# Optimization experiments

Measured on AMD Instinct MI355X. Metric: run time of the kernel, lower is better.

The kernel has to match this reference:

```python
import jax, jax.numpy as jnp
import numpy as np

L, B, F, E, H, V, NL, K = 32, 128, 4096, 512, 512, 50000, 2, 20


def setup_inputs() -> dict:
    key = jax.random.key(0)
    ks = jax.random.split(key, 9)
    return {
        "dialog_encoder_inputs": jax.random.randint(ks[0], (L, B), 0, V),
        "fact_inputs": jax.random.normal(ks[1], (B, F, E), dtype=jnp.float32),
        "h": jax.random.normal(ks[2], (NL, B, H), dtype=jnp.float32),
        "c": jax.random.normal(ks[3], (NL, B, H), dtype=jnp.float32),
        "enc_emb": jax.random.normal(ks[4], (V, E), dtype=jnp.float32) * 0.02,
        "Aw": jax.random.normal(ks[5], (H, E), dtype=jnp.float32) * 0.04,
        "Ab": jnp.zeros((H,), dtype=jnp.float32),
        "Cw": jax.random.normal(ks[6], (H, E), dtype=jnp.float32) * 0.04,
        "Cb": jnp.zeros((H,), dtype=jnp.float32),
        "top_k": K,
    }


def reference(dialog_encoder_inputs, fact_inputs, h, c, enc_emb, Aw, Ab, Cw, Cb, top_k):
    # --- get_top_k_fact_average: embed dialog, score facts, gather top-k ---
    q = enc_emb[dialog_encoder_inputs].mean(axis=0)                # [B, E] mean-pooled query
    scores = jnp.einsum('be,bfe->bf', q, fact_inputs)              # [B, F] similarity
    _, idx = jax.lax.top_k(scores, top_k)                          # [B, K]
    topf = jnp.take_along_axis(fact_inputs, idx[:, :, None], axis=1)  # [B, K, E]

    # --- facts_forward: memory-network style hidden-state update ---
    fact_M = jnp.einsum('bke,he->bkh', topf, Aw) + Ab              # fact_linearA
    fact_C = jnp.einsum('bke,he->bkh', topf, Cw) + Cb              # fact_linearC

    def update(u):  # u: [NL, B, H]
        P = jax.nn.softmax(jnp.einsum('bke,lbe->lbk', topf, u), axis=-1)  # attn over facts
        o = jnp.einsum('lbk,bke->lbe', P, topf)                           # weighted fact avg
        return o + u

    return update(h), update(c), fact_M, fact_C
```

## Files before the change

### kernel.cpp

```cpp
#include <hip/hip_runtime.h>
#include <float.h>
#include <math.h>

#define LL 32
#define BB 128
#define FF 4096
#define EE 512
#define HH 512
#define NLAYER 2
#define KK 20

typedef float f4 __attribute__((ext_vector_type(4)));
typedef short bf16x8 __attribute__((ext_vector_type(8)));
typedef float f32x4 __attribute__((ext_vector_type(4)));

__device__ inline unsigned short bf16rne(float x) {
    unsigned u = __float_as_uint(x);
    u += 0x7fff + ((u >> 16) & 1);
    return (unsigned short)(u >> 16);
}

__global__ __launch_bounds__(256) void prep_kernel(const int* __restrict__ tok,
                                                   const float* __restrict__ emb,
                                                   float* __restrict__ q,
                                                   const float* __restrict__ Aw,
                                                   const float* __restrict__ Cw,
                                                   unsigned short* __restrict__ Wbf) {
    int bid = blockIdx.x;
    if (bid < 256) {
        int b = bid >> 1, eh = bid & 1;
        __shared__ int ts[LL];
        if (threadIdx.x < LL) ts[threadIdx.x] = tok[threadIdx.x * BB + b];
        __syncthreads();
        int e = eh * 256 + threadIdx.x;
        float acc = 0.f;
        #pragma unroll
        for (int l = 0; l < LL; ++l) acc += emb[(long)ts[l] * EE + e];
        q[b * EE + e] = acc * (1.0f / LL);
    } else {
        int cid = bid - 256;
        int matY = cid >> 8;
        int blkX = cid & 255;
        const float* W = matY ? Cw : Aw;
        unsigned short* dst = Wbf + (size_t)matY * HH * EE;
        int i = (blkX * 256 + threadIdx.x) * 4;
        float4 v = *(const float4*)(W + i);
        ushort4 o;
        o.x = bf16rne(v.x); o.y = bf16rne(v.y); o.z = bf16rne(v.z); o.w = bf16rne(v.w);
        *(ushort4*)(dst + i) = o;
    }
}

__global__ __launch_bounds__(256) void scores_kernel(const float* __restrict__ q,
                                                     const float* __restrict__ fact,
                                                     float* __restrict__ scores) {
    int b = blockIdx.y;
    int wave = threadIdx.x >> 6;
    int lane = threadIdx.x & 63;
    const f4* qv = (const f4*)(q + b * EE);
    f4 qa = qv[lane];
    f4 qb = qv[64 + lane];
    int f0 = (blockIdx.x * 4 + wave) * 8;
    float d[8];
    #pragma unroll
    for (int i = 0; i < 8; ++i) {
        const f4* fv = (const f4*)(fact + ((long)b * FF + f0 + i) * EE);
        f4 fa = __builtin_nontemporal_load(fv + lane);
        f4 fb = __builtin_nontemporal_load(fv + 64 + lane);
        f4 p = qa * fa + qb * fb;
        d[i] = p.x + p.y + p.z + p.w;
    }
    bool h32 = lane & 32;
    float e0, e1, e2, e3;
    {
        float s0 = __shfl_xor(d[0], 32), s1 = __shfl_xor(d[1], 32);
        float s2 = __shfl_xor(d[2], 32), s3 = __shfl_xor(d[3], 32);
        float s4 = __shfl_xor(d[4], 32), s5 = __shfl_xor(d[5], 32);
        float s6 = __shfl_xor(d[6], 32), s7 = __shfl_xor(d[7], 32);
        e0 = h32 ? d[4] + s4 : d[0] + s0;
        e1 = h32 ? d[5] + s5 : d[1] + s1;
        e2 = h32 ? d[6] + s6 : d[2] + s2;
        e3 = h32 ? d[7] + s7 : d[3] + s3;
    }
    bool h16 = lane & 16;
    float g0, g1;
    {
        float s0 = __shfl_xor(e0, 16), s1 = __shfl_xor(e1, 16);
        float s2 = __shfl_xor(e2, 16), s3 = __shfl_xor(e3, 16);
        g0 = h16 ? e2 + s2 : e0 + s0;
        g1 = h16 ? e3 + s3 : e1 + s1;
    }
    bool h8 = lane & 8;
    float hs;
    {
        float s0 = __shfl_xor(g0, 8), s1 = __shfl_xor(g1, 8);
        hs = h8 ? g1 + s1 : g0 + s0;
    }
    hs += __shfl_xor(hs, 4);
    hs += __shfl_xor(hs, 2);
    hs += __shfl_xor(hs, 1);
    if ((lane & 7) == 0) scores[b * FF + f0 + ((lane >> 3) & 7)] = hs;
}

__global__ __launch_bounds__(256) void topk_update_kernel(const float* __restrict__ scores,
                                                          const float* __restrict__ fact,
                                                          const float* __restrict__ hin,
                                                          const float* __restrict__ cin,
                                                          unsigned short* __restrict__ topfb,
                                                          float* __restrict__ out) {
    int b = blockIdx.x;
    __shared__ float tf[KK][EE];
    __shared__ unsigned long long wbest[4];
    __shared__ unsigned long long wkey_s;
    __shared__ int sel[KK];
    int t = threadIdx.x;
    int wave = t >> 6, lane = t & 63;

    unsigned long long keys[16];
    {
        const float4* sv = (const float4*)(scores + b * FF);
        #pragma unroll
        for (int s = 0; s < 4; ++s) {
            float4 v = sv[t + 256 * s];
            float vc[4] = {v.x, v.y, v.z, v.w};
            #pragma unroll
            for (int c = 0; c < 4; ++c) {
                int idx = 4 * (t + 256 * s) + c;
                unsigned u = __float_as_uint(vc[c]);
                u ^= ((int)u >> 31) | 0x80000000u;
                keys[s * 4 + c] = ((unsigned long long)u << 32) | (unsigned)(FF - 1 - idx);
            }
        }
    }

    for (int it = 0; it < KK; ++it) {
        unsigned long long best = keys[0];
        #pragma unroll
        for (int i = 1; i < 16; ++i) best = keys[i] > best ? keys[i] : best;
        #pragma unroll
        for (int off = 32; off > 0; off >>= 1) {
            unsigned long long o = __shfl_xor(best, off, 64);
            if (o > best) best = o;
        }
        if (lane == 0) wbest[wave] = best;
        __syncthreads();
        if (t == 0) {
            unsigned long long bb = wbest[0];
            if (wbest[1] > bb) bb = wbest[1];
            if (wbest[2] > bb) bb = wbest[2];
            if (wbest[3] > bb) bb = wbest[3];
            wkey_s = bb;
            sel[it] = FF - 1 - (int)(bb & 0xFFFFFFFFu);
        }
        __syncthreads();
        unsigned long long wk = wkey_s;
        #pragma unroll
        for (int i = 0; i < 16; ++i)
            if (keys[i] == wk) keys[i] = 0;
    }

    for (int kk = 0; kk < KK; kk += 2) {
        int k = kk + (t >> 7);
        int e = t & 127;
        int src = sel[k];
        float4 v = *(const float4*)(fact + (((long)b * FF + src) * EE) + e * 4);
        *(float4*)&tf[k][e * 4] = v;
        ushort4 o;
        o.x = bf16rne(v.x); o.y = bf16rne(v.y); o.z = bf16rne(v.z); o.w = bf16rne(v.w);
        *(ushort4*)(topfb + ((size_t)b * KK + k) * EE + e * 4) = o;
    }
    __syncthreads();

    const float* u = (wave < 2 ? hin : cin) + ((size_t)(wave & 1) * BB + b) * EE;
    const float4* uv = (const float4*)u;
    float4 ua = uv[lane], ub = uv[64 + lane];
    float sk[KK];
    #pragma unroll
    for (int k = 0; k < KK; ++k) {
        const float4* tv = (const float4*)&tf[k][0];
        float4 ta = tv[lane], tb = tv[64 + lane];
        float d = ua.x * ta.x + ua.y * ta.y + ua.z * ta.z + ua.w * ta.w
                + ub.x * tb.x + ub.y * tb.y + ub.z * tb.z + ub.w * tb.w;
        #pragma unroll
        for (int off = 32; off > 0; off >>= 1) d += __shfl_xor(d, off, 64);
        sk[k] = d;
    }
    float m = sk[0];
    #pragma unroll
    for (int k = 1; k < KK; ++k) m = fmaxf(m, sk[k]);
    float sum = 0.f;
    #pragma unroll
    for (int k = 0; k < KK; ++k) { sk[k] = __expf(sk[k] - m); sum += sk[k]; }
    float inv = 1.f / sum;
    float4 oa = {0, 0, 0, 0}, ob = {0, 0, 0, 0};
    #pragma unroll
    for (int k = 0; k < KK; ++k) {
        float p = sk[k] * inv;
        const float4* tv = (const float4*)&tf[k][0];
        float4 ta = tv[lane], tb = tv[64 + lane];
        oa.x += p * ta.x; oa.y += p * ta.y; oa.z += p * ta.z; oa.w += p * ta.w;
        ob.x += p * tb.x; ob.y += p * tb.y; ob.z += p * tb.z; ob.w += p * tb.w;
    }
    oa.x += ua.x; oa.y += ua.y; oa.z += ua.z; oa.w += ua.w;
    ob.x += ub.x; ob.y += ub.y; ob.z += ub.z; ob.w += ub.w;
    float* obase = out + (size_t)(wave < 2 ? 0 : NLAYER * BB * HH)
                       + ((size_t)(wave & 1) * BB + b) * HH;
    float4* ov = (float4*)obase;
    ov[lane] = oa;
    ov[64 + lane] = ob;
}

__global__ __launch_bounds__(256) void factmc_kernel(const unsigned short* __restrict__ topfb,
                                                     const unsigned short* __restrict__ Wbf,
                                                     const float* __restrict__ Ab,
                                                     const float* __restrict__ Cb,
                                                     float* __restrict__ out) {
    int b = blockIdx.x, mat = blockIdx.y;
    const unsigned short* W = Wbf + (size_t)mat * HH * EE;
    const float* bias = mat ? Cb : Ab;
    float* O = out + (size_t)2 * NLAYER * BB * HH
                   + (size_t)mat * BB * KK * HH + (size_t)b * KK * HH;

    __shared__ unsigned short tf[32 * EE];
    {
        const unsigned short* src = topfb + (size_t)b * KK * EE;
        for (int ib = threadIdx.x; ib < KK * EE / 8; ib += 256) {
            int row = ib >> 6;
            int cb = ib & 63;
            float4 v = *(const float4*)(src + row * EE + cb * 8);
            int byte = (row * 1024 + cb * 16) ^ ((row & 7) << 4);
            *(float4*)((char*)tf + byte) = v;
        }
    }
    __syncthreads();

    int wave = threadIdx.x >> 6, lane = threadIdx.x & 63;
    int lrow = lane & 15, lk = lane >> 4;
    f32x4 acc[2][8];
    #pragma unroll
    for (int m = 0; m < 2; ++m)
        #pragma unroll
        for (int n = 0; n < 8; ++n) acc[m][n] = (f32x4){0, 0, 0, 0};

    const unsigned short* wbase = W + (size_t)(wave * 128 + lrow) * EE + lk * 8;

    #pragma unroll 2
    for (int ks = 0; ks < 16; ++ks) {
        int col2 = (ks * 32 + lk * 8) * 2;
        int byte0 = (lrow * 1024 + col2) ^ ((lrow & 7) << 4);
        bf16x8 a0 = *(const bf16x8*)((const char*)tf + byte0);
        int r1 = 16 + lrow;
        int byte1 = (r1 * 1024 + col2) ^ ((r1 & 7) << 4);
        bf16x8 a1 = *(const bf16x8*)((const char*)tf + byte1);
        #pragma unroll
        for (int n = 0; n < 8; ++n) {
            bf16x8 bfrag = *(const bf16x8*)(wbase + (size_t)n * 16 * EE + ks * 32);
            acc[0][n] = __builtin_amdgcn_mfma_f32_16x16x32_bf16(a0, bfrag, acc[0][n], 0, 0, 0);
            acc[1][n] = __builtin_amdgcn_mfma_f32_16x16x32_bf16(a1, bfrag, acc[1][n], 0, 0, 0);
        }
    }

    #pragma unroll
    for (int n = 0; n < 8; ++n) {
        int h = wave * 128 + n * 16 + lrow;
        float bv = bias[h];
        #pragma unroll
        for (int r = 0; r < 4; ++r) {
            int k0 = lk * 4 + r;
            O[(size_t)k0 * HH + h] = acc[0][n][r] + bv;
            int k1 = 16 + lk * 4 + r;
            if (k1 < KK) O[(size_t)k1 * HH + h] = acc[1][n][r] + bv;
        }
    }
}

extern "C" void kernel_launch(void* const* d_in, const int* in_sizes, int n_in,
                              void* d_out, int out_size, void* d_ws, size_t ws_size,
                              hipStream_t stream) {
    const int* tok = (const int*)d_in[0];
    const float* fact = (const float*)d_in[1];
    const float* hin = (const float*)d_in[2];
    const float* cin = (const float*)d_in[3];
    const float* emb = (const float*)d_in[4];
    const float* Aw = (const float*)d_in[5];
    const float* Ab = (const float*)d_in[6];
    const float* Cw = (const float*)d_in[7];
    const float* Cb = (const float*)d_in[8];
    float* out = (float*)d_out;

    float* ws = (float*)d_ws;
    float* q = ws;
    float* scores = ws + 65536;
    unsigned short* topfb = (unsigned short*)(ws + 65536 + 524288);
    unsigned short* Wbf = (unsigned short*)(ws + 65536 + 524288 + 655360);

    prep_kernel<<<768, 256, 0, stream>>>(tok, emb, q, Aw, Cw, Wbf);
    scores_kernel<<<dim3(FF / 32, BB), 256, 0, stream>>>(q, fact, scores);
    topk_update_kernel<<<BB, 256, 0, stream>>>(scores, fact, hin, cin, topfb, out);
    factmc_kernel<<<dim3(BB, 2), 256, 0, stream>>>(topfb, Wbf, Ab, Cb, out);
}
```

Measured before the change: 220.5 us.

## Fuse scoring and top-k into one kernel with per-chunk candidates and last-block merge

Merges the score and top-k/update kernels into one. Each block scores a 128-fact chunk, keeps its local top-20 in shared memory and writes them as candidates, and the last block per batch row (found with an atomic counter) merges the 640 candidates and runs the fact update. This removes the full scores round trip through global memory and one launch, and replaces the 4096-wide per-row top-k with a two-level selection. In exchange, each block now holds a large shared tf buffer, which may lower occupancy for the bandwidth-bound scoring phase, and the merge step rests on atomics and a threadfence.

```diff
diff --git a/kernel.cpp b/kernel.cpp
--- a/kernel.cpp
+++ b/kernel.cpp
@@ -20,12 +20,19 @@
     return (unsigned short)(u >> 16);
 }
 
+__device__ inline unsigned long long packkey(float v, int fidx) {
+    unsigned u = __float_as_uint(v);
+    u ^= ((int)u >> 31) | 0x80000000u;
+    return ((unsigned long long)u << 32) | (unsigned)(FF - 1 - fidx);
+}
+
 __global__ __launch_bounds__(256) void prep_kernel(const int* __restrict__ tok,
                                                    const float* __restrict__ emb,
                                                    float* __restrict__ q,
                                                    const float* __restrict__ Aw,
                                                    const float* __restrict__ Cw,
-                                                   unsigned short* __restrict__ Wbf) {
+                                                   unsigned short* __restrict__ Wbf,
+                                                   int* __restrict__ counter) {
     int bid = blockIdx.x;
     if (bid < 256) {
         int b = bid >> 1, eh = bid & 1;
@@ -37,7 +44,7 @@
         #pragma unroll
         for (int l = 0; l < LL; ++l) acc += emb[(long)ts[l] * EE + e];
         q[b * EE + e] = acc * (1.0f / LL);
-    } else {
+    } else if (bid < 768) {
         int cid = bid - 256;
         int matY = cid >> 8;
         int blkX = cid & 255;
@@ -48,119 +55,125 @@
         ushort4 o;
         o.x = bf16rne(v.x); o.y = bf16rne(v.y); o.z = bf16rne(v.z); o.w = bf16rne(v.w);
         *(ushort4*)(dst + i) = o;
-    }
-}
-
-__global__ __launch_bounds__(256) void scores_kernel(const float* __restrict__ q,
-                                                     const float* __restrict__ fact,
-                                                     float* __restrict__ scores) {
-    int b = blockIdx.y;
-    int wave = threadIdx.x >> 6;
-    int lane = threadIdx.x & 63;
+    } else {
+        if (threadIdx.x < BB) counter[threadIdx.x] = 0;
+    }
+}
+
+__global__ __launch_bounds__(256) void scores_topk_kernel(const float* __restrict__ q,
+                                                          const float* __restrict__ fact,
+                                                          const float* __restrict__ hin,
+                                                          const float* __restrict__ cin,
+                                                          unsigned long long* __restrict__ cand,
+                                                          int* __restrict__ counter,
+                                                          unsigned short* __restrict__ topfb,
+                                                          float* __restrict__ out) {
+    int b = blockIdx.y, chunk = blockIdx.x;
+    __shared__ float ssc[128];
+    __shared__ float tf[KK][EE];
+    __shared__ int sel[KK];
+    __shared__ int flag;
+    int t = threadIdx.x;
+    int wave = t >> 6, lane = t & 63;
+
     const f4* qv = (const f4*)(q + b * EE);
     f4 qa = qv[lane];
     f4 qb = qv[64 + lane];
-    int f0 = (blockIdx.x * 4 + wave) * 8;
-    float d[8];
-    #pragma unroll
-    for (int i = 0; i < 8; ++i) {
-        const f4* fv = (const f4*)(fact + ((long)b * FF + f0 + i) * EE);
-        f4 fa = __builtin_nontemporal_load(fv + lane);
-        f4 fb = __builtin_nontemporal_load(fv + 64 + lane);
-        f4 p = qa * fa + qb * fb;
-        d[i] = p.x + p.y + p.z + p.w;
-    }
-    bool h32 = lane & 32;
-    float e0, e1, e2, e3;
-    {
-        float s0 = __shfl_xor(d[0], 32), s1 = __shfl_xor(d[1], 32);
-        float s2 = __shfl_xor(d[2], 32), s3 = __shfl_xor(d[3], 32);
-        float s4 = __shfl_xor(d[4], 32), s5 = __shfl_xor(d[5], 32);
-        float s6 = __shfl_xor(d[6], 32), s7 = __shfl_xor(d[7], 32);
-        e0 = h32 ? d[4] + s4 : d[0] + s0;
-        e1 = h32 ? d[5] + s5 : d[1] + s1;
-        e2 = h32 ? d[6] + s6 : d[2] + s2;
-        e3 = h32 ? d[7] + s7 : d[3] + s3;
-    }
-    bool h16 = lane & 16;
-    float g0, g1;
-    {
-        float s0 = __shfl_xor(e0, 16), s1 = __shfl_xor(e1, 16);
-        float s2 = __shfl_xor(e2, 16), s3 = __shfl_xor(e3, 16);
-        g0 = h16 ? e2 + s2 : e0 + s0;
-        g1 = h16 ? e3 + s3 : e1 + s1;
-    }
-    bool h8 = lane & 8;
-    float hs;
-    {
-        float s0 = __shfl_xor(g0, 8), s1 = __shfl_xor(g1, 8);
-        hs = h8 ? g1 + s1 : g0 + s0;
-    }
-    hs += __shfl_xor(hs, 4);
-    hs += __shfl_xor(hs, 2);
-    hs += __shfl_xor(hs, 1);
-    if ((lane & 7) == 0) scores[b * FF + f0 + ((lane >> 3) & 7)] = hs;
-}
-
-__global__ __launch_bounds__(256) void topk_update_kernel(const float* __restrict__ scores,
-                                                          const float* __restrict__ fact,
-                                                          const float* __restrict__ hin,
-                                                          const float* __restrict__ cin,
-                                                          unsigned short* __restrict__ topfb,
-                                                          float* __restrict__ out) {
-    int b = blockIdx.x;
-    __shared__ float tf[KK][EE];
-    __shared__ unsigned long long wbest[4];
-    __shared__ unsigned long long wkey_s;
-    __shared__ int sel[KK];
-    int t = threadIdx.x;
-    int wave = t >> 6, lane = t & 63;
-
-    unsigned long long keys[16];
-    {
-        const float4* sv = (const float4*)(scores + b * FF);
-        #pragma unroll
-        for (int s = 0; s < 4; ++s) {
-            float4 v = sv[t + 256 * s];
-            float vc[4] = {v.x, v.y, v.z, v.w};
+
+    for (int it = 0; it < 4; ++it) {
+        int f0 = chunk * 128 + wave * 32 + it * 8;
+        float d[8];
+        #pragma unroll
+        for (int i = 0; i < 8; ++i) {
+            const f4* fv = (const f4*)(fact + ((long)b * FF + f0 + i) * EE);
+            f4 fa = __builtin_nontemporal_load(fv + lane);
+            f4 fb = __builtin_nontemporal_load(fv + 64 + lane);
+            f4 p = qa * fa + qb * fb;
+            d[i] = p.x + p.y + p.z + p.w;
+        }
+        bool h32 = lane & 32;
+        float e0, e1, e2, e3;
+        {
+            float s0 = __shfl_xor(d[0], 32), s1 = __shfl_xor(d[1], 32);
+            float s2 = __shfl_xor(d[2], 32), s3 = __shfl_xor(d[3], 32);
+            float s4 = __shfl_xor(d[4], 32), s5 = __shfl_xor(d[5], 32);
+            float s6 = __shfl_xor(d[6], 32), s7 = __shfl_xor(d[7], 32);
+            e0 = h32 ? d[4] + s4 : d[0] + s0;
+            e1 = h32 ? d[5] + s5 : d[1] + s1;
+            e2 = h32 ? d[6] + s6 : d[2] + s2;
+            e3 = h32 ? d[7] + s7 : d[3] + s3;
+        }
+        bool h16 = lane & 16;
+        float g0, g1;
+        {
+            float s0 = __shfl_xor(e0, 16), s1 = __shfl_xor(e1, 16);
+            float s2 = __shfl_xor(e2, 16), s3 = __shfl_xor(e3, 16);
+            g0 = h16 ? e2 + s2 : e0 + s0;
+            g1 = h16 ? e3 + s3 : e1 + s1;
+        }
+        bool h8 = lane & 8;
+        float hs;
+        {
+            float s0 = __shfl_xor(g0, 8), s1 = __shfl_xor(g1, 8);
+            hs = h8 ? g1 + s1 : g0 + s0;
+        }
+        hs += __shfl_xor(hs, 4);
+        hs += __shfl_xor(hs, 2);
+        hs += __shfl_xor(hs, 1);
+        if ((lane & 7) == 0) ssc[wave * 32 + it * 8 + ((lane >> 3) & 7)] = hs;
+    }
+    __syncthreads();
+
+    if (wave == 0) {
+        unsigned long long k0 = packkey(ssc[lane], chunk * 128 + lane);
+        unsigned long long k1 = packkey(ssc[64 + lane], chunk * 128 + 64 + lane);
+        unsigned long long mykey = 0;
+        for (int it = 0; it < KK; ++it) {
+            unsigned long long best = k0 > k1 ? k0 : k1;
             #pragma unroll
-            for (int c = 0; c < 4; ++c) {
-                int idx = 4 * (t + 256 * s) + c;
-                unsigned u = __float_as_uint(vc[c]);
-                u ^= ((int)u >> 31) | 0x80000000u;
-                keys[s * 4 + c] = ((unsigned long long)u << 32) | (unsigned)(FF - 1 - idx);
+            for (int off = 32; off > 0; off >>= 1) {
+                unsigned long long o = __shfl_xor(best, off, 64);
+                if (o > best) best = o;
             }
-        }
-    }
-
-    for (int it = 0; it < KK; ++it) {
-        unsigned long long best = keys[0];
-        #pragma unroll
-        for (int i = 1; i < 16; ++i) best = keys[i] > best ? keys[i] : best;
-        #pragma unroll
-        for (int off = 32; off > 0; off >>= 1) {
-            unsigned long long o = __shfl_xor(best, off, 64);
-            if (o > best) best = o;
-        }
-        if (lane == 0) wbest[wave] = best;
-        __syncthreads();
-        if (t == 0) {
-            unsigned long long bb = wbest[0];
-            if (wbest[1] > bb) bb = wbest[1];
-            if (wbest[2] > bb) bb = wbest[2];
-            if (wbest[3] > bb) bb = wbest[3];
-            wkey_s = bb;
-            sel[it] = FF - 1 - (int)(bb & 0xFFFFFFFFu);
-        }
-        __syncthreads();
-        unsigned long long wk = wkey_s;
-        #pragma unroll
-        for (int i = 0; i < 16; ++i)
-            if (keys[i] == wk) keys[i] = 0;
-    }
-
-    for (int kk = 0; kk < KK; kk += 2) {
-        int k = kk + (t >> 7);
+            if (lane == it) mykey = best;
+            if (k0 == best) k0 = 0;
+            if (k1 == best) k1 = 0;
+        }
+        if (lane < KK) cand[((size_t)b * 32 + chunk) * KK + lane] = mykey;
+        __threadfence();
+        if (lane == 0) {
+            int old = atomicAdd(&counter[b], 1);
+            flag = (old == 31);
+        }
+    }
+    __syncthreads();
+    if (!flag) return;
+
+    if (wave == 0) {
+        __threadfence();
+        unsigned long long kk[10];
+        #pragma unroll
+        for (int i = 0; i < 10; ++i)
+            kk[i] = cand[(size_t)b * 640 + i * 64 + lane];
+        for (int it = 0; it < KK; ++it) {
+            unsigned long long best = kk[0];
+            #pragma unroll
+            for (int i = 1; i < 10; ++i) best = kk[i] > best ? kk[i] : best;
+            #pragma unroll
+            for (int off = 32; off > 0; off >>= 1) {
+                unsigned long long o = __shfl_xor(best, off, 64);
+                if (o > best) best = o;
+            }
+            if (lane == 0) sel[it] = FF - 1 - (int)(best & 0xFFFFFFFFu);
+            #pragma unroll
+            for (int i = 0; i < 10; ++i)
+                if (kk[i] == best) kk[i] = 0;
+        }
+    }
+    __syncthreads();
+
+    for (int kk2 = 0; kk2 < KK; kk2 += 2) {
+        int k = kk2 + (t >> 7);
         int e = t & 127;
         int src = sel[k];
         float4 v = *(const float4*)(fact + (((long)b * FF + src) * EE) + e * 4);
@@ -290,12 +303,12 @@
 
     float* ws = (float*)d_ws;
     float* q = ws;
-    float* scores = ws + 65536;
-    unsigned short* topfb = (unsigned short*)(ws + 65536 + 524288);
-    unsigned short* Wbf = (unsigned short*)(ws + 65536 + 524288 + 655360);
-
-    prep_kernel<<<768, 256, 0, stream>>>(tok, emb, q, Aw, Cw, Wbf);
-    scores_kernel<<<dim3(FF / 32, BB), 256, 0, stream>>>(q, fact, scores);
-    topk_update_kernel<<<BB, 256, 0, stream>>>(scores, fact, hin, cin, topfb, out);
+    unsigned long long* cand = (unsigned long long*)(ws + 65536);
+    int* counter = (int*)(ws + 65536 + 163840);
+    unsigned short* topfb = (unsigned short*)(ws + 65536 + 163840 + 128);
+    unsigned short* Wbf = (unsigned short*)(ws + 65536 + 163840 + 128 + 655360);
+
+    prep_kernel<<<769, 256, 0, stream>>>(tok, emb, q, Aw, Cw, Wbf, counter);
+    scores_topk_kernel<<<dim3(32, BB), 256, 0, stream>>>(q, fact, hin, cin, cand, counter, topfb, out);
     factmc_kernel<<<dim3(BB, 2), 256, 0, stream>>>(topfb, Wbf, Ab, Cb, out);
 }
```

New measurement: 465.1 us. +110.9%, slower.
